# Kernel tuning notes

Hardware: AMD Instinct MI355X
Metric: run time of the kernel (lower is better)

The kernel has to match this reference:

```python
import jax, jax.numpy as jnp
import numpy as np

N_NODES = 50000
N_EDGES = 800000
F_IN = 64
HID = 64
N_CLASSES = 10


def setup_inputs() -> dict:
    key = jax.random.key(0)
    ks = jax.random.split(key, 16)
    features = jax.random.normal(ks[0], (N_NODES, F_IN), dtype=jnp.float32)
    edge_indicies = jax.random.randint(ks[1], (2, N_EDGES), 0, N_NODES, dtype=jnp.int64)
    s = 1.0 / np.sqrt(HID)
    params = {}
    # three GINConv MLPs: Linear(in,64) -> ReLU -> Linear(64,64)
    for i in range(3):
        d_in = F_IN if i == 0 else HID
        si = 1.0 / np.sqrt(d_in)
        params[f"W1_{i}"] = jax.random.uniform(ks[2 + 4 * i], (d_in, HID), jnp.float32, -si, si)
        params[f"b1_{i}"] = jax.random.uniform(ks[3 + 4 * i], (HID,), jnp.float32, -si, si)
        params[f"W2_{i}"] = jax.random.uniform(ks[4 + 4 * i], (HID, HID), jnp.float32, -s, s)
        params[f"b2_{i}"] = jax.random.uniform(ks[5 + 4 * i], (HID,), jnp.float32, -s, s)
    params["W_lin"] = jax.random.uniform(ks[14], (HID, N_CLASSES), jnp.float32, -s, s)
    params["b_lin"] = jax.random.uniform(ks[15], (N_CLASSES,), jnp.float32, -s, s)
    return {"features": features, "edge_indicies": edge_indicies, **params}


def _gin_conv(x, src, dst, W1, b1, W2, b2):
    # aggregate: sum_{j in N(i)} x_j  (messages flow src -> dst), eps = 0
    agg = jax.ops.segment_sum(x[src], dst, num_segments=N_NODES)
    h = agg + x  # (1 + eps) * x + aggregate, eps=0
    # MLP: Linear -> ReLU -> Linear
    return jax.nn.relu(h @ W1 + b1) @ W2 + b2


def reference(features, edge_indicies,
              W1_0, b1_0, W2_0, b2_0,
              W1_1, b1_1, W2_1, b2_1,
              W1_2, b1_2, W2_2, b2_2,
              W_lin, b_lin):
    src, dst = edge_indicies[0], edge_indicies[1]
    x = jax.nn.relu(_gin_conv(features, src, dst, W1_0, b1_0, W2_0, b2_0))
    x = jax.nn.relu(_gin_conv(x, src, dst, W1_1, b1_1, W2_1, b2_1))
    x = jax.nn.relu(_gin_conv(x, src, dst, W1_2, b1_2, W2_2, b2_2))
    return x @ W_lin + b_lin
```

## Files before the change

kernel.cpp:

```cpp
#include <hip/hip_runtime.h>
#include <hip/hip_bf16.h>

#define FDIM 64
#define BNODES 64
#define CHUNK 4096
#define HP 72
#define GCAP 2048

typedef short bf16x8 __attribute__((ext_vector_type(8)));
typedef float f32x4 __attribute__((ext_vector_type(4)));

__device__ __forceinline__ unsigned short f2bf(float f) {
    unsigned int u = __float_as_uint(f);
    unsigned int r = (u + 0x7fffu + ((u >> 16) & 1u)) >> 16;
    return (unsigned short)r;
}
__device__ __forceinline__ float bflo(unsigned int p) { return __uint_as_float(p << 16); }
__device__ __forceinline__ float bfhi(unsigned int p) { return __uint_as_float(p & 0xffff0000u); }

__global__ __launch_bounds__(256) void cast_prep_hist(const float* __restrict__ x,
                                                      unsigned short* __restrict__ xb, int n4,
                                                      int ncast,
                                                      const float* __restrict__ W10,
                                                      const float* __restrict__ W20,
                                                      const float* __restrict__ W11,
                                                      const float* __restrict__ W21,
                                                      const float* __restrict__ W12,
                                                      const float* __restrict__ W22,
                                                      unsigned short* __restrict__ wt,
                                                      const int* __restrict__ dst,
                                                      int* __restrict__ hist,
                                                      int n_edges, int nbuck) {
    int tid = threadIdx.x;
    if (blockIdx.x < (unsigned)ncast) {
        int i = blockIdx.x * 256 + tid;
        if (i < n4) {
            float4 v = ((const float4*)x)[i];
            uint2 o;
            o.x = (unsigned int)f2bf(v.x) | ((unsigned int)f2bf(v.y) << 16);
            o.y = (unsigned int)f2bf(v.z) | ((unsigned int)f2bf(v.w) << 16);
            ((uint2*)xb)[i] = o;
        }
        return;
    }
    if (blockIdx.x < (unsigned)(ncast + 6)) {
        __shared__ unsigned short s[64 * 64];
        int wsel = blockIdx.x - ncast;
        const float* W;
        switch (wsel) {
            case 0: W = W10; break;
            case 1: W = W20; break;
            case 2: W = W11; break;
            case 3: W = W21; break;
            case 4: W = W12; break;
            default: W = W22; break;
        }
#pragma unroll
        for (int p = 0; p < 4; p++) {
            int idx = tid + p * 256;
            int k = idx >> 4;
            int n0 = (idx & 15) * 4;
            float4 v = ((const float4*)W)[idx];
            s[(n0 + 0) * 64 + k] = f2bf(v.x);
            s[(n0 + 1) * 64 + k] = f2bf(v.y);
            s[(n0 + 2) * 64 + k] = f2bf(v.z);
            s[(n0 + 3) * 64 + k] = f2bf(v.w);
        }
        __syncthreads();
        uint4* o = (uint4*)(wt + (size_t)wsel * 4096);
#pragma unroll
        for (int p = 0; p < 2; p++) {
            int idx = tid + p * 256;
            o[idx] = ((uint4*)s)[idx];
        }
        return;
    }
    {
        __shared__ int lh[1024];
        int chunk = blockIdx.x - ncast - 6;
        for (int i = tid; i < nbuck; i += 256) lh[i] = 0;
        __syncthreads();
        int beg = chunk * CHUNK;
        int end = min(beg + CHUNK, n_edges);
        for (int e = beg + tid; e < end; e += 256)
            atomicAdd(&lh[dst[e] >> 6], 1);
        __syncthreads();
        for (int i = tid; i < nbuck; i += 256)
            hist[(size_t)chunk * nbuck + i] = lh[i];
    }
}

__global__ __launch_bounds__(256) void scan_chunks(const int* __restrict__ hist,
                                                   int* __restrict__ chunk_off,
                                                   int* __restrict__ bucket_total,
                                                   int nchunks, int nbuck) {
    __shared__ int s[256];
    int b = blockIdx.x;
    int t = threadIdx.x;
    int v = (t < nchunks) ? hist[(size_t)t * nbuck + b] : 0;
    s[t] = v;
    __syncthreads();
    for (int off = 1; off < 256; off <<= 1) {
        int u = (t >= off) ? s[t - off] : 0;
        __syncthreads();
        s[t] += u;
        __syncthreads();
    }
    if (t < nchunks) chunk_off[(size_t)t * nbuck + b] = s[t] - v;
    if (t == 255) bucket_total[b] = s[255];
}

__global__ __launch_bounds__(1024) void scan_buckets(const int* __restrict__ bucket_total,
                                                     int* __restrict__ bucket_start,
                                                     int* __restrict__ row_ptr,
                                                     int nbuck, int n_nodes, int n_edges) {
    __shared__ int s[1024];
    int t = threadIdx.x;
    int v = (t < nbuck) ? bucket_total[t] : 0;
    s[t] = v;
    __syncthreads();
    for (int off = 1; off < 1024; off <<= 1) {
        int u = (t >= off) ? s[t - off] : 0;
        __syncthreads();
        s[t] += u;
        __syncthreads();
    }
    if (t < nbuck) bucket_start[t] = s[t] - v;
    if (t == 0) { bucket_start[nbuck] = n_edges; row_ptr[n_nodes] = n_edges; }
}

__global__ __launch_bounds__(256) void bucket_fill(const int* __restrict__ src,
                                                   const int* __restrict__ dst,
                                                   const int* __restrict__ bucket_start,
                                                   const int* __restrict__ chunk_off,
                                                   unsigned int* __restrict__ packed,
                                                   int n_edges, int nbuck) {
    __shared__ int cur[1024];
    int chunk = blockIdx.x;
    for (int i = threadIdx.x; i < nbuck; i += 256)
        cur[i] = bucket_start[i] + chunk_off[(size_t)chunk * nbuck + i];
    __syncthreads();
    int beg = chunk * CHUNK;
    int end = min(beg + CHUNK, n_edges);
    for (int e = beg + threadIdx.x; e < end; e += 256) {
        int d = dst[e];
        int b = d >> 6;
        int pos = atomicAdd(&cur[b], 1);
        packed[pos] = (unsigned int)src[e] | ((unsigned int)(d & 63) << 16);
    }
}

#define ACCUM(v0, v1)                                          \
    acc[0] += bflo((v0).x); acc[1] += bfhi((v0).x);            \
    acc[2] += bflo((v0).y); acc[3] += bfhi((v0).y);            \
    acc[4] += bflo((v0).z); acc[5] += bfhi((v0).z);            \
    acc[6] += bflo((v0).w); acc[7] += bfhi((v0).w);            \
    acc[8] += bflo((v1).x); acc[9] += bfhi((v1).x);            \
    acc[10] += bflo((v1).y); acc[11] += bfhi((v1).y);          \
    acc[12] += bflo((v1).z); acc[13] += bfhi((v1).z);          \
    acc[14] += bflo((v1).w); acc[15] += bfhi((v1).w);

__global__ __launch_bounds__(256) void conv_fused(
        const unsigned short* __restrict__ xb,
        const unsigned int* __restrict__ packed,
        const int* __restrict__ bucket_start,
        int* __restrict__ src_sorted,
        int* __restrict__ row_ptr,
        const unsigned short* __restrict__ wt1, const float* __restrict__ b1,
        const unsigned short* __restrict__ wt2, const float* __restrict__ b2,
        const float* __restrict__ Wl, const float* __restrict__ bl,
        unsigned short* __restrict__ y, float* __restrict__ out,
        int n_nodes, int do_sort, int do_final) {
    __shared__ __align__(16) unsigned char ubuf[16384];
    unsigned int* spk = (unsigned int*)ubuf;
    int* sidx = (int*)(ubuf + 8192);
    unsigned short* sH = (unsigned short*)ubuf;
    __shared__ int cnt[BNODES], nbeg[BNODES], cur[BNODES];
    __shared__ float sWl[FDIM * 10];
    __shared__ float sbl[16];

    int b = blockIdx.x;
    int tid = threadIdx.x;
    int base = b * BNODES;

    if (do_final) {
        for (int i = tid; i < FDIM * 10; i += 256) sWl[i] = Wl[i];
        if (tid < 10) sbl[tid] = bl[tid];
    }

    int nl = tid >> 2;
    int node = base + nl;
    bool valid = node < n_nodes;
    int q = (tid & 3) * 16;

    int ebeg, total, dbeg = 0, dcnt = 0;
    bool fits;

    if (do_sort) {
        ebeg = bucket_start[b];
        int eend = bucket_start[b + 1];
        total = eend - ebeg;
        fits = (total <= GCAP);
        if (tid < BNODES) cnt[tid] = 0;
        if (fits)
            for (int i = tid; i < total; i += 256) spk[i] = packed[ebeg + i];
        __syncthreads();
        if (fits) {
            for (int i = tid; i < total; i += 256) atomicAdd(&cnt[spk[i] >> 16], 1);
        } else {
            for (int e = ebeg + tid; e < eend; e += 256) atomicAdd(&cnt[packed[e] >> 16], 1);
        }
        __syncthreads();
        if (tid < 64) {
            int v = cnt[tid];
            int inc = v;
#pragma unroll
            for (int off = 1; off < 64; off <<= 1) {
                int u = __shfl_up(inc, off, 64);
                if (tid >= off) inc += u;
            }
            int ex = inc - v;
            nbeg[tid] = ex;
            cur[tid] = ex;
            int nd = base + tid;
            if (nd < n_nodes) row_ptr[nd] = ebeg + ex;
        }
        __syncthreads();
        if (fits) {
            for (int i = tid; i < total; i += 256) {
                unsigned int p = spk[i];
                int pos = atomicAdd(&cur[p >> 16], 1);
                int s = (int)(p & 0xFFFFu);
                sidx[pos] = s;
                src_sorted[ebeg + pos] = s;
            }
        } else {
            for (int e = ebeg + tid; e < eend; e += 256) {
                unsigned int p = packed[e];
                int pos = atomicAdd(&cur[p >> 16], 1);
                src_sorted[ebeg + pos] = (int)(p & 0xFFFFu);
            }
        }
        __syncthreads();
        dbeg = nbeg[nl];
        dcnt = cnt[nl];
    } else {
        ebeg = row_ptr[base];
        int eend = row_ptr[min(base + BNODES, n_nodes)];
        total = eend - ebeg;
        fits = (total <= GCAP);
        int stage = fits ? total : GCAP;
        for (int i = tid; i < stage; i += 256) sidx[i] = src_sorted[ebeg + i];
        int rb = valid ? row_ptr[node] : ebeg;
        int re = valid ? row_ptr[node + 1] : ebeg;
        dbeg = rb - ebeg;
        dcnt = re - rb;
        __syncthreads();
    }

    int dend = dbeg + dcnt;
    int dmid;
    if (fits) dmid = dend;
    else if (do_sort) dmid = dbeg;
    else dmid = min(dend, GCAP);

    float acc[16];
    if (valid) {
        const uint4* xr = (const uint4*)(xb + (size_t)node * FDIM + q);
        uint4 v0 = xr[0], v1 = xr[1];
        acc[0] = bflo(v0.x); acc[1] = bfhi(v0.x);
        acc[2] = bflo(v0.y); acc[3] = bfhi(v0.y);
        acc[4] = bflo(v0.z); acc[5] = bfhi(v0.z);
        acc[6] = bflo(v0.w); acc[7] = bfhi(v0.w);
        acc[8] = bflo(v1.x); acc[9] = bfhi(v1.x);
        acc[10] = bflo(v1.y); acc[11] = bfhi(v1.y);
        acc[12] = bflo(v1.z); acc[13] = bfhi(v1.z);
        acc[14] = bflo(v1.w); acc[15] = bfhi(v1.w);
    } else {
#pragma unroll
        for (int i = 0; i < 16; i++) acc[i] = 0.f;
    }

    int e = dbeg;
    for (; e + 3 < dmid; e += 4) {
        int s[4];
#pragma unroll
        for (int j = 0; j < 4; j++) s[j] = sidx[e + j];
        uint4 va[4], vb[4];
#pragma unroll
        for (int j = 0; j < 4; j++) {
            const uint4* p = (const uint4*)(xb + (size_t)s[j] * FDIM + q);
            va[j] = p[0];
            vb[j] = p[1];
        }
#pragma unroll
        for (int j = 0; j < 4; j++) { ACCUM(va[j], vb[j]); }
    }
    for (; e < dmid; e++) {
        const uint4* p = (const uint4*)(xb + (size_t)sidx[e] * FDIM + q);
        uint4 v0 = p[0], v1 = p[1];
        ACCUM(v0, v1);
    }
    for (; e < dend; e++) {
        const uint4* p = (const uint4*)(xb + (size_t)src_sorted[ebeg + e] * FDIM + q);
        uint4 v0 = p[0], v1 = p[1];
        ACCUM(v0, v1);
    }

    __syncthreads();

    {
        uint4 p0, p1;
        p0.x = (unsigned int)f2bf(acc[0]) | ((unsigned int)f2bf(acc[1]) << 16);
        p0.y = (unsigned int)f2bf(acc[2]) | ((unsigned int)f2bf(acc[3]) << 16);
        p0.z = (unsigned int)f2bf(acc[4]) | ((unsigned int)f2bf(acc[5]) << 16);
        p0.w = (unsigned int)f2bf(acc[6]) | ((unsigned int)f2bf(acc[7]) << 16);
        p1.x = (unsigned int)f2bf(acc[8]) | ((unsigned int)f2bf(acc[9]) << 16);
        p1.y = (unsigned int)f2bf(acc[10]) | ((unsigned int)f2bf(acc[11]) << 16);
        p1.z = (unsigned int)f2bf(acc[12]) | ((unsigned int)f2bf(acc[13]) << 16);
        p1.w = (unsigned int)f2bf(acc[14]) | ((unsigned int)f2bf(acc[15]) << 16);
        *(uint4*)(&sH[nl * HP + q]) = p0;
        *(uint4*)(&sH[nl * HP + q + 8]) = p1;
    }
    __syncthreads();

    int w = tid >> 6;
    int lane = tid & 63;
    int qd = lane >> 4;
    int m = lane & 15;
    int arow = (w * 16 + m) * HP;

    f32x4 a4[4];

    {
        bf16x8 a0 = *(bf16x8*)(&sH[arow + qd * 8]);
        bf16x8 a1 = *(bf16x8*)(&sH[arow + 32 + qd * 8]);
#pragma unroll
        for (int t = 0; t < 4; t++) {
            float bias = b1[t * 16 + m];
            a4[t] = (f32x4){bias, bias, bias, bias};
            bf16x8 bA = *(const bf16x8*)(wt1 + (size_t)(t * 16 + m) * FDIM + qd * 8);
            bf16x8 bB = *(const bf16x8*)(wt1 + (size_t)(t * 16 + m) * FDIM + 32 + qd * 8);
            a4[t] = __builtin_amdgcn_mfma_f32_16x16x32_bf16(a0, bA, a4[t], 0, 0, 0);
            a4[t] = __builtin_amdgcn_mfma_f32_16x16x32_bf16(a1, bB, a4[t], 0, 0, 0);
        }
#pragma unroll
        for (int t = 0; t < 4; t++)
#pragma unroll
            for (int r = 0; r < 4; r++)
                sH[(w * 16 + qd * 4 + r) * HP + t * 16 + m] = f2bf(fmaxf(a4[t][r], 0.f));
    }

    {
        bf16x8 a0 = *(bf16x8*)(&sH[arow + qd * 8]);
        bf16x8 a1 = *(bf16x8*)(&sH[arow + 32 + qd * 8]);
#pragma unroll
        for (int t = 0; t < 4; t++) {
            float bias = b2[t * 16 + m];
            a4[t] = (f32x4){bias, bias, bias, bias};
            bf16x8 bA = *(const bf16x8*)(wt2 + (size_t)(t * 16 + m) * FDIM + qd * 8);
            bf16x8 bB = *(const bf16x8*)(wt2 + (size_t)(t * 16 + m) * FDIM + 32 + qd * 8);
            a4[t] = __builtin_amdgcn_mfma_f32_16x16x32_bf16(a0, bA, a4[t], 0, 0, 0);
            a4[t] = __builtin_amdgcn_mfma_f32_16x16x32_bf16(a1, bB, a4[t], 0, 0, 0);
        }
#pragma unroll
        for (int t = 0; t < 4; t++)
#pragma unroll
            for (int r = 0; r < 4; r++)
                sH[(w * 16 + qd * 4 + r) * HP + t * 16 + m] = f2bf(fmaxf(a4[t][r], 0.f));
    }
    __syncthreads();

    if (!do_final) {
#pragma unroll
        for (int p = 0; p < 2; p++) {
            int idx = tid + p * 256;
            int r = idx >> 3, qq = idx & 7;
            if (base + r < n_nodes)
                *(uint4*)(y + (size_t)(base + r) * FDIM + qq * 8) = *(uint4*)(&sH[r * HP + qq * 8]);
        }
    } else {
        for (int i = tid; i < 64 * 10; i += 256) {
            int n2 = i / 10, cc = i % 10;
            int nd = base + n2;
            if (nd < n_nodes) {
                float s = sbl[cc];
#pragma unroll
                for (int k0 = 0; k0 < FDIM; k0 += 4) {
                    uint2 hp = *(uint2*)(&sH[n2 * HP + k0]);
                    s += bflo(hp.x) * sWl[(k0 + 0) * 10 + cc] + bfhi(hp.x) * sWl[(k0 + 1) * 10 + cc]
                       + bflo(hp.y) * sWl[(k0 + 2) * 10 + cc] + bfhi(hp.y) * sWl[(k0 + 3) * 10 + cc];
                }
                out[(size_t)nd * 10 + cc] = s;
            }
        }
    }
}

extern "C" void kernel_launch(void* const* d_in, const int* in_sizes, int n_in,
                              void* d_out, int out_size, void* d_ws, size_t ws_size,
                              hipStream_t stream) {
    const float* features = (const float*)d_in[0];
    const int* edges = (const int*)d_in[1];
    int n_nodes = in_sizes[0] / FDIM;
    int n_edges = in_sizes[1] / 2;
    const int* src = edges;
    const int* dst = edges + n_edges;

    int nbuck = (n_nodes + BNODES - 1) / BNODES;
    int nchunks = (n_edges + CHUNK - 1) / CHUNK;

    int* hist = (int*)d_ws;
    int* chunk_off = hist + (size_t)nchunks * nbuck;
    int* bucket_total = chunk_off + (size_t)nchunks * nbuck;
    int* bucket_start = bucket_total + nbuck;
    int* row_ptr = bucket_start + nbuck + 1;
    unsigned int* packed = (unsigned int*)(row_ptr + n_nodes + 1);
    int* src_sorted = (int*)(packed + n_edges);
    size_t int_elems = 2 * (size_t)nchunks * nbuck + 2 * (size_t)nbuck + 2
                       + (size_t)n_nodes + 2 * (size_t)n_edges;
    int_elems = (int_elems + 3) & ~(size_t)3;
    size_t buf_elems = (size_t)n_nodes * FDIM;
    unsigned short* hb  = (unsigned short*)((int*)d_ws + int_elems);
    unsigned short* xb0 = hb + buf_elems;
    unsigned short* yA  = xb0 + buf_elems;
    unsigned short* yB  = yA + buf_elems;
    unsigned short* wt  = yB + buf_elems;
    (void)hb;

    dim3 bs(256);
    int n4 = (int)(buf_elems / 4);
    int ncast = (n4 + 255) / 256;
    dim3 gs_cph(ncast + 6 + nchunks);

    cast_prep_hist<<<gs_cph, bs, 0, stream>>>(features, xb0, n4, ncast,
                                              (const float*)d_in[2], (const float*)d_in[4],
                                              (const float*)d_in[6], (const float*)d_in[8],
                                              (const float*)d_in[10], (const float*)d_in[12], wt,
                                              dst, hist, n_edges, nbuck);

    scan_chunks<<<nbuck, 256, 0, stream>>>(hist, chunk_off, bucket_total, nchunks, nbuck);
    scan_buckets<<<1, 1024, 0, stream>>>(bucket_total, bucket_start, row_ptr, nbuck, n_nodes, n_edges);
    bucket_fill<<<nchunks, 256, 0, stream>>>(src, dst, bucket_start, chunk_off, packed, n_edges, nbuck);

    const float* Wl = (const float*)d_in[14];
    const float* bl = (const float*)d_in[15];

    conv_fused<<<nbuck, bs, 0, stream>>>(xb0, packed, bucket_start, src_sorted, row_ptr,
                                         wt, (const float*)d_in[3],
                                         wt + 4096, (const float*)d_in[5],
                                         Wl, bl, yA, (float*)d_out, n_nodes, 1, 0);

    conv_fused<<<nbuck, bs, 0, stream>>>(yA, packed, bucket_start, src_sorted, row_ptr,
                                         wt + 2 * 4096, (const float*)d_in[7],
                                         wt + 3 * 4096, (const float*)d_in[9],
                                         Wl, bl, yB, (float*)d_out, n_nodes, 0, 0);

    conv_fused<<<nbuck, bs, 0, stream>>>(yB, packed, bucket_start, src_sorted, row_ptr,
                                         wt + 4 * 4096, (const float*)d_in[11],
                                         wt + 5 * 4096, (const float*)d_in[13],
                                         Wl, bl, yA, (float*)d_out, n_nodes, 0, 1);
}
```

Before: 193.1 us.

## Use 512 threads per block with 8 lanes per node in GIN conv

```diff
diff --git a/kernel.cpp b/kernel.cpp
--- a/kernel.cpp
+++ b/kernel.cpp
@@ -6,6 +6,7 @@
 #define CHUNK 4096
 #define HP 72
 #define GCAP 2048
+#define CVT 512
 
 typedef short bf16x8 __attribute__((ext_vector_type(8)));
 typedef float f32x4 __attribute__((ext_vector_type(4)));
@@ -150,20 +151,16 @@
     }
 }
 
-#define ACCUM(v0, v1)                                          \
-    acc[0] += bflo((v0).x); acc[1] += bfhi((v0).x);            \
-    acc[2] += bflo((v0).y); acc[3] += bfhi((v0).y);            \
-    acc[4] += bflo((v0).z); acc[5] += bfhi((v0).z);            \
-    acc[6] += bflo((v0).w); acc[7] += bfhi((v0).w);            \
-    acc[8] += bflo((v1).x); acc[9] += bfhi((v1).x);            \
-    acc[10] += bflo((v1).y); acc[11] += bfhi((v1).y);          \
-    acc[12] += bflo((v1).z); acc[13] += bfhi((v1).z);          \
-    acc[14] += bflo((v1).w); acc[15] += bfhi((v1).w);
-
-__global__ __launch_bounds__(256) void conv_fused(
-        const unsigned short* __restrict__ xb,
+#define ACCUM8(v)                                              \
+    acc[0] += bflo((v).x); acc[1] += bfhi((v).x);              \
+    acc[2] += bflo((v).y); acc[3] += bfhi((v).y);              \
+    acc[4] += bflo((v).z); acc[5] += bfhi((v).z);              \
+    acc[6] += bflo((v).w); acc[7] += bfhi((v).w);
+
+__global__ __launch_bounds__(CVT) void conv_fused(
         const unsigned int* __restrict__ packed,
         const int* __restrict__ bucket_start,
+        const unsigned short* __restrict__ xb,
         int* __restrict__ src_sorted,
         int* __restrict__ row_ptr,
         const unsigned short* __restrict__ wt1, const float* __restrict__ b1,
@@ -184,14 +181,14 @@
     int base = b * BNODES;
 
     if (do_final) {
-        for (int i = tid; i < FDIM * 10; i += 256) sWl[i] = Wl[i];
+        for (int i = tid; i < FDIM * 10; i += CVT) sWl[i] = Wl[i];
         if (tid < 10) sbl[tid] = bl[tid];
     }
 
-    int nl = tid >> 2;
+    int nl = tid >> 3;
     int node = base + nl;
     bool valid = node < n_nodes;
-    int q = (tid & 3) * 16;
+    int q = (tid & 7) * 8;
 
     int ebeg, total, dbeg = 0, dcnt = 0;
     bool fits;
@@ -203,12 +200,12 @@
         fits = (total <= GCAP);
         if (tid < BNODES) cnt[tid] = 0;
         if (fits)
-            for (int i = tid; i < total; i += 256) spk[i] = packed[ebeg + i];
+            for (int i = tid; i < total; i += CVT) spk[i] = packed[ebeg + i];
         __syncthreads();
         if (fits) {
-            for (int i = tid; i < total; i += 256) atomicAdd(&cnt[spk[i] >> 16], 1);
+            for (int i = tid; i < total; i += CVT) atomicAdd(&cnt[spk[i] >> 16], 1);
         } else {
-            for (int e = ebeg + tid; e < eend; e += 256) atomicAdd(&cnt[packed[e] >> 16], 1);
+            for (int e = ebeg + tid; e < eend; e += CVT) atomicAdd(&cnt[packed[e] >> 16], 1);
         }
         __syncthreads();
         if (tid < 64) {
@@ -227,7 +224,7 @@
         }
         __syncthreads();
         if (fits) {
-            for (int i = tid; i < total; i += 256) {
+            for (int i = tid; i < total; i += CVT) {
                 unsigned int p = spk[i];
                 int pos = atomicAdd(&cur[p >> 16], 1);
                 int s = (int)(p & 0xFFFFu);
@@ -235,7 +232,7 @@
                 src_sorted[ebeg + pos] = s;
             }
         } else {
-            for (int e = ebeg + tid; e < eend; e += 256) {
+            for (int e = ebeg + tid; e < eend; e += CVT) {
                 unsigned int p = packed[e];
                 int pos = atomicAdd(&cur[p >> 16], 1);
                 src_sorted[ebeg + pos] = (int)(p & 0xFFFFu);
@@ -250,7 +247,7 @@
         total = eend - ebeg;
         fits = (total <= GCAP);
         int stage = fits ? total : GCAP;
-        for (int i = tid; i < stage; i += 256) sidx[i] = src_sorted[ebeg + i];
+        for (int i = tid; i < stage; i += CVT) sidx[i] = src_sorted[ebeg + i];
         int rb = valid ? row_ptr[node] : ebeg;
         int re = valid ? row_ptr[node + 1] : ebeg;
         dbeg = rb - ebeg;
@@ -264,63 +261,60 @@
     else if (do_sort) dmid = dbeg;
     else dmid = min(dend, GCAP);
 
-    float acc[16];
+    float acc[8];
     if (valid) {
-        const uint4* xr = (const uint4*)(xb + (size_t)node * FDIM + q);
-        uint4 v0 = xr[0], v1 = xr[1];
-        acc[0] = bflo(v0.x); acc[1] = bfhi(v0.x);
-        acc[2] = bflo(v0.y); acc[3] = bfhi(v0.y);
-        acc[4] = bflo(v0.z); acc[5] = bfhi(v0.z);
-        acc[6] = bflo(v0.w); acc[7] = bfhi(v0.w);
-        acc[8] = bflo(v1.x); acc[9] = bfhi(v1.x);
-        acc[10] = bflo(v1.y); acc[11] = bfhi(v1.y);
-        acc[12] = bflo(v1.z); acc[13] = bfhi(v1.z);
-        acc[14] = bflo(v1.w); acc[15] = bfhi(v1.w);
+        uint4 v = *(const uint4*)(xb + (size_t)node * FDIM + q);
+        acc[0] = bflo(v.x); acc[1] = bfhi(v.x);
+        acc[2] = bflo(v.y); acc[3] = bfhi(v.y);
+        acc[4] = bflo(v.z); acc[5] = bfhi(v.z);
+        acc[6] = bflo(v.w); acc[7] = bfhi(v.w);
     } else {
 #pragma unroll
-        for (int i = 0; i < 16; i++) acc[i] = 0.f;
+        for (int i = 0; i < 8; i++) acc[i] = 0.f;
     }
 
     int e = dbeg;
-    for (; e + 3 < dmid; e += 4) {
+    for (; e + 7 < dmid; e += 8) {
+        int s[8];
+#pragma unroll
+        for (int j = 0; j < 8; j++) s[j] = sidx[e + j];
+        uint4 v[8];
+#pragma unroll
+        for (int j = 0; j < 8; j++) v[j] = *(const uint4*)(xb + (size_t)s[j] * FDIM + q);
+#pragma unroll
+        for (int j = 0; j < 8; j++) { ACCUM8(v[j]); }
+    }
+    if (e + 3 < dmid) {
         int s[4];
 #pragma unroll
         for (int j = 0; j < 4; j++) s[j] = sidx[e + j];
-        uint4 va[4], vb[4];
-#pragma unroll
-        for (int j = 0; j < 4; j++) {
-            const uint4* p = (const uint4*)(xb + (size_t)s[j] * FDIM + q);
-            va[j] = p[0];
-            vb[j] = p[1];
-        }
-#pragma unroll
-        for (int j = 0; j < 4; j++) { ACCUM(va[j], vb[j]); }
+        uint4 v[4];
+#pragma unroll
+        for (int j = 0; j < 4; j++) v[j] = *(const uint4*)(xb + (size_t)s[j] * FDIM + q);
+#pragma unroll
+        for (int j = 0; j < 4; j++) { ACCUM8(v[j]); }
+        e += 4;
     }
     for (; e < dmid; e++) {
-        const uint4* p = (const uint4*)(xb + (size_t)sidx[e] * FDIM + q);
-        uint4 v0 = p[0], v1 = p[1];
-        ACCUM(v0, v1);
+        uint4 v = *(const uint4*)(xb + (size_t)sidx[e] * FDIM + q);
+        ACCUM8(v);
     }
     for (; e < dend; e++) {
-        const uint4* p = (const uint4*)(xb + (size_t)src_sorted[ebeg + e] * FDIM + q);
-        uint4 v0 = p[0], v1 = p[1];
-        ACCUM(v0, v1);
+        uint4 v = *(const uint4*)(xb + (size_t)src_sorted[ebeg + e] * FDIM + q);
+        ACCUM8(v);
     }
 
     __syncthreads();
 
     {
-        uint4 p0, p1;
+        uint2 p0;
         p0.x = (unsigned int)f2bf(acc[0]) | ((unsigned int)f2bf(acc[1]) << 16);
         p0.y = (unsigned int)f2bf(acc[2]) | ((unsigned int)f2bf(acc[3]) << 16);
-        p0.z = (unsigned int)f2bf(acc[4]) | ((unsigned int)f2bf(acc[5]) << 16);
-        p0.w = (unsigned int)f2bf(acc[6]) | ((unsigned int)f2bf(acc[7]) << 16);
-        p1.x = (unsigned int)f2bf(acc[8]) | ((unsigned int)f2bf(acc[9]) << 16);
-        p1.y = (unsigned int)f2bf(acc[10]) | ((unsigned int)f2bf(acc[11]) << 16);
-        p1.z = (unsigned int)f2bf(acc[12]) | ((unsigned int)f2bf(acc[13]) << 16);
-        p1.w = (unsigned int)f2bf(acc[14]) | ((unsigned int)f2bf(acc[15]) << 16);
-        *(uint4*)(&sH[nl * HP + q]) = p0;
-        *(uint4*)(&sH[nl * HP + q + 8]) = p1;
+        uint2 p1;
+        p1.x = (unsigned int)f2bf(acc[4]) | ((unsigned int)f2bf(acc[5]) << 16);
+        p1.y = (unsigned int)f2bf(acc[6]) | ((unsigned int)f2bf(acc[7]) << 16);
+        *(uint2*)(&sH[nl * HP + q]) = p0;
+        *(uint2*)(&sH[nl * HP + q + 4]) = p1;
     }
     __syncthreads();
 
@@ -328,59 +322,63 @@
     int lane = tid & 63;
     int qd = lane >> 4;
     int m = lane & 15;
-    int arow = (w * 16 + m) * HP;
-
-    f32x4 a4[4];
+    int rowblk = w & 3;
+    int tp = (w >> 2) * 2;
+    int arow = (rowblk * 16 + m) * HP;
+
+    f32x4 a4[2];
 
     {
         bf16x8 a0 = *(bf16x8*)(&sH[arow + qd * 8]);
         bf16x8 a1 = *(bf16x8*)(&sH[arow + 32 + qd * 8]);
-#pragma unroll
-        for (int t = 0; t < 4; t++) {
+        __syncthreads();
+#pragma unroll
+        for (int tt = 0; tt < 2; tt++) {
+            int t = tp + tt;
             float bias = b1[t * 16 + m];
-            a4[t] = (f32x4){bias, bias, bias, bias};
+            a4[tt] = (f32x4){bias, bias, bias, bias};
             bf16x8 bA = *(const bf16x8*)(wt1 + (size_t)(t * 16 + m) * FDIM + qd * 8);
             bf16x8 bB = *(const bf16x8*)(wt1 + (size_t)(t * 16 + m) * FDIM + 32 + qd * 8);
-            a4[t] = __builtin_amdgcn_mfma_f32_16x16x32_bf16(a0, bA, a4[t], 0, 0, 0);
-            a4[t] = __builtin_amdgcn_mfma_f32_16x16x32_bf16(a1, bB, a4[t], 0, 0, 0);
-        }
-#pragma unroll
-        for (int t = 0; t < 4; t++)
+            a4[tt] = __builtin_amdgcn_mfma_f32_16x16x32_bf16(a0, bA, a4[tt], 0, 0, 0);
+            a4[tt] = __builtin_amdgcn_mfma_f32_16x16x32_bf16(a1, bB, a4[tt], 0, 0, 0);
+        }
+#pragma unroll
+        for (int tt = 0; tt < 2; tt++)
 #pragma unroll
             for (int r = 0; r < 4; r++)
-                sH[(w * 16 + qd * 4 + r) * HP + t * 16 + m] = f2bf(fmaxf(a4[t][r], 0.f));
-    }
+                sH[(rowblk * 16 + qd * 4 + r) * HP + (tp + tt) * 16 + m] = f2bf(fmaxf(a4[tt][r], 0.f));
+    }
+    __syncthreads();
 
     {
         bf16x8 a0 = *(bf16x8*)(&sH[arow + qd * 8]);
         bf16x8 a1 = *(bf16x8*)(&sH[arow + 32 + qd * 8]);
-#pragma unroll
-        for (int t = 0; t < 4; t++) {
+        __syncthreads();
+#pragma unroll
+        for (int tt = 0; tt < 2; tt++) {
+            int t = tp + tt;
             float bias = b2[t * 16 + m];
-            a4[t] = (f32x4){bias, bias, bias, bias};
+            a4[tt] = (f32x4){bias, bias, bias, bias};
             bf16x8 bA = *(const bf16x8*)(wt2 + (size_t)(t * 16 + m) * FDIM + qd * 8);
             bf16x8 bB = *(const bf16x8*)(wt2 + (size_t)(t * 16 + m) * FDIM + 32 + qd * 8);
-            a4[t] = __builtin_amdgcn_mfma_f32_16x16x32_bf16(a0, bA, a4[t], 0, 0, 0);
-            a4[t] = __builtin_amdgcn_mfma_f32_16x16x32_bf16(a1, bB, a4[t], 0, 0, 0);
-        }
-#pragma unroll
-        for (int t = 0; t < 4; t++)
+            a4[tt] = __builtin_amdgcn_mfma_f32_16x16x32_bf16(a0, bA, a4[tt], 0, 0, 0);
+            a4[tt] = __builtin_amdgcn_mfma_f32_16x16x32_bf16(a1, bB, a4[tt], 0, 0, 0);
+        }
+#pragma unroll
+        for (int tt = 0; tt < 2; tt++)
 #pragma unroll
             for (int r = 0; r < 4; r++)
-                sH[(w * 16 + qd * 4 + r) * HP + t * 16 + m] = f2bf(fmaxf(a4[t][r], 0.f));
+                sH[(rowblk * 16 + qd * 4 + r) * HP + (tp + tt) * 16 + m] = f2bf(fmaxf(a4[tt][r], 0.f));
     }
     __syncthreads();
 
     if (!do_final) {
-#pragma unroll
-        for (int p = 0; p < 2; p++) {
-            int idx = tid + p * 256;
-            int r = idx >> 3, qq = idx & 7;
-            if (base + r < n_nodes)
-                *(uint4*)(y + (size_t)(base + r) * FDIM + qq * 8) = *(uint4*)(&sH[r * HP + qq * 8]);
-        }
+        int idx = tid;
+        int r = idx >> 3, qq = idx & 7;
+        if (base + r < n_nodes)
+            *(uint4*)(y + (size_t)(base + r) * FDIM + qq * 8) = *(uint4*)(&sH[r * HP + qq * 8]);
     } else {
-        for (int i = tid; i < 64 * 10; i += 256) {
+        for (int i = tid; i < 64 * 10; i += CVT) {
             int n2 = i / 10, cc = i % 10;
             int nd = base + n2;
             if (nd < n_nodes) {
@@ -421,12 +419,10 @@
                        + (size_t)n_nodes + 2 * (size_t)n_edges;
     int_elems = (int_elems + 3) & ~(size_t)3;
     size_t buf_elems = (size_t)n_nodes * FDIM;
-    unsigned short* hb  = (unsigned short*)((int*)d_ws + int_elems);
-    unsigned short* xb0 = hb + buf_elems;
+    unsigned short* xb0 = (unsigned short*)((int*)d_ws + int_elems);
     unsigned short* yA  = xb0 + buf_elems;
     unsigned short* yB  = yA + buf_elems;
     unsigned short* wt  = yB + buf_elems;
-    (void)hb;
 
     dim3 bs(256);
     int n4 = (int)(buf_elems / 4);
@@ -446,18 +442,18 @@
     const float* Wl = (const float*)d_in[14];
     const float* bl = (const float*)d_in[15];
 
-    conv_fused<<<nbuck, bs, 0, stream>>>(xb0, packed, bucket_start, src_sorted, row_ptr,
-                                         wt, (const float*)d_in[3],
-                                         wt + 4096, (const float*)d_in[5],
-                                         Wl, bl, yA, (float*)d_out, n_nodes, 1, 0);
-
-    conv_fused<<<nbuck, bs, 0, stream>>>(yA, packed, bucket_start, src_sorted, row_ptr,
-                                         wt + 2 * 4096, (const float*)d_in[7],
-                                         wt + 3 * 4096, (const float*)d_in[9],
-                                         Wl, bl, yB, (float*)d_out, n_nodes, 0, 0);
-
-    conv_fused<<<nbuck, bs, 0, stream>>>(yB, packed, bucket_start, src_sorted, row_ptr,
-                                         wt + 4 * 4096, (const float*)d_in[11],
-                                         wt + 5 * 4096, (const float*)d_in[13],
-                                         Wl, bl, yA, (float*)d_out, n_nodes, 0, 1);
-}
+    conv_fused<<<nbuck, CVT, 0, stream>>>(packed, bucket_start, xb0, src_sorted, row_ptr,
+                                          wt, (const float*)d_in[3],
+                                          wt + 4096, (const float*)d_in[5],
+                                          Wl, bl, yA, (float*)d_out, n_nodes, 1, 0);
+
+    conv_fused<<<nbuck, CVT, 0, stream>>>(packed, bucket_start, yA, src_sorted, row_ptr,
+                                          wt + 2 * 4096, (const float*)d_in[7],
+                                          wt + 3 * 4096, (const float*)d_in[9],
+                                          Wl, bl, yB, (float*)d_out, n_nodes, 0, 0);
+
+    conv_fused<<<nbuck, CVT, 0, stream>>>(packed, bucket_start, yB, src_sorted, row_ptr,
+                                          wt + 4 * 4096, (const float*)d_in[11],
+                                          wt + 5 * 4096, (const float*)d_in[13],
+                                          Wl, bl, yA, (float*)d_out, n_nodes, 0, 1);
+}
```

New measurement: 199.1 us. 3.1% more time.
